# Performance work log

Measured on AMD Instinct MI355X. Metric: run time of the kernel, lower is better.

Reference implementation:

```python
import jax, jax.numpy as jnp
import numpy as np

B, L, M = 256, 8, 1024  # batch, input_length (= window), latent dim m
P = 8                   # predict_length


def setup_inputs() -> dict:
    key = jax.random.key(0)
    k1, k2, k3 = jax.random.split(key, 3)
    x = jax.random.normal(k1, (B, L, M), dtype=jnp.float32)
    # A initialized near identity (original init is torch.eye repeated), plus
    # small noise so the test is non-trivial and the recurrence stays stable.
    eye = jnp.broadcast_to(jnp.eye(M, dtype=jnp.float32), (L, M, M))
    A_real = eye / L + 0.02 * jax.random.normal(k2, (L, M, M), dtype=jnp.float32)
    A_imag = 0.02 * jax.random.normal(k3, (L, M, M), dtype=jnp.float32)
    return {"x": x, "A_real": A_real, "A_imag": A_imag, "predict_length": P}


def reference(x, A_real, A_imag, predict_length):
    # Complex DMD operator bank: A[j] is [M, M] cfloat.
    A = (A_real + 1j * A_imag).astype(jnp.complex64)
    Lw = x.shape[1]
    # Original inner loop: u2 += A[j] @ uc[:, -j]  (note -0 == 0!)
    #   j=0 pairs A[0] with window position 0; j>=1 pairs A[j] with position Lw-j.
    # Re-index so term for window position p uses Ag[p]: Ag[0]=A[0], Ag[p]=A[Lw-p].
    idx = jnp.concatenate([jnp.array([0]), jnp.arange(Lw - 1, 0, -1)])
    Ag = A[idx]  # [Lw, M, M]

    uc0 = x.astype(jnp.complex64)  # [B, Lw, M] sliding window state

    def step(uc, _):
        # Fused accumulation: sum_p Ag[p] @ uc[:, p]  -> [B, M]
        u2 = jnp.einsum("kmn,bkn->bm", Ag, uc)
        uc = jnp.concatenate([uc[:, 1:], u2[:, None]], axis=1)  # slide window
        return uc, None

    uc, _ = jax.lax.scan(step, uc0, None, length=predict_length)
    # Original casts cfloat -> double, which drops the imaginary part; keep fp32.
    return jnp.real(uc).astype(jnp.float32)
```

## Files before the change

### kernel.cpp

```cpp
#include <hip/hip_runtime.h>


#define LW 8

typedef __attribute__((ext_vector_type(8))) short  short8;
typedef __attribute__((ext_vector_type(8))) __bf16 bf16x8;
typedef __attribute__((ext_vector_type(4))) float  f32x4;
typedef __attribute__((ext_vector_type(4))) float  f4;
typedef const __attribute__((address_space(1))) void gvoid_t;
typedef __attribute__((address_space(3))) void lvoid_t;

static __device__ __forceinline__ short f2bf(float f) {
  unsigned u = __builtin_bit_cast(unsigned, f);
  u += 0x7FFFu + ((u >> 16) & 1u);
  return (short)(u >> 16);
}
static __device__ __forceinline__ float bf2f(short s) {
  unsigned u = ((unsigned)(unsigned short)s) << 16;
  return __builtin_bit_cast(float, u);
}
static __device__ __forceinline__ f32x4 mfma16(short8 a, short8 b, f32x4 c) {
  return __builtin_amdgcn_mfma_f32_16x16x32_bf16(
      __builtin_bit_cast(bf16x8, a), __builtin_bit_cast(bf16x8, b), c, 0, 0, 0);
}

__global__ __launch_bounds__(1024) void prep_all(const float* __restrict__ x,
                                                 const float* __restrict__ Ar,
                                                 const float* __restrict__ Ai,
                                                 short* __restrict__ Sr2,
                                                 short* __restrict__ Si2,
                                                 short* __restrict__ Wr5,
                                                 short* __restrict__ Wi5) {
  const int bid = blockIdx.x;
  if (bid < 1024) {
    const int tg = bid * 1024 + threadIdx.x;
    const int sq = tg & 3, col = (tg >> 2) & 31, kcg = (tg >> 7) & 31;
    const int colt = (tg >> 12) & 31, p = tg >> 17;
    const int qn = sq ^ ((col >> 1) & 3);
    const int m = (colt << 5) + col, n0 = (kcg << 5) + (qn << 3);
    const int qm = (LW - p) & 7;
    const size_t src = ((size_t)((qm << 10) + m) << 10) + n0;
    f4 r0 = *(const f4*)(Ar + src), r1 = *(const f4*)(Ar + src + 4);
    f4 i0 = *(const f4*)(Ai + src), i1 = *(const f4*)(Ai + src + 4);
    short8 vr, vi;
#pragma unroll
    for (int j = 0; j < 4; ++j) {
      vr[j] = f2bf(r0[j]); vr[j + 4] = f2bf(r1[j]);
      vi[j] = f2bf(i0[j]); vi[j + 4] = f2bf(i1[j]);
    }
    *(short8*)(Wr5 + ((size_t)tg << 3)) = vr;
    *(short8*)(Wi5 + ((size_t)tg << 3)) = vi;
  } else {
    const int tg = (bid - 1024) * 1024 + threadIdx.x;
    const int qn = tg & 3, kc = (tg >> 2) & 31, b = (tg >> 7) & 255, s = tg >> 15;
    const float* xp = x + ((size_t)(b * LW + s) << 10) + (kc << 5) + (qn << 3);
    f4 x0 = *(const f4*)xp, x1 = *(const f4*)(xp + 4);
    short8 v;
#pragma unroll
    for (int j = 0; j < 4; ++j) { v[j] = f2bf(x0[j]); v[j + 4] = f2bf(x1[j]); }
    const int sq = qn ^ ((b >> 1) & 3);
    const size_t dst = ((size_t)s << 18) + (kc << 13) + (b << 5) + (sq << 3);
    *(short8*)(Sr2 + dst) = v;
    short8 z = {0, 0, 0, 0, 0, 0, 0, 0};
    *(short8*)(Si2 + dst) = z;
  }
}


#define LOADA(set_, kc_) do {                                                    \
    const int kg_ = ((ks << 4) + (kc_)) << 13;                                   \
    _Pragma("unroll")                                                            \
    for (int rf_ = 0; rf_ < 4; ++rf_) {                                          \
      aR[set_][rf_] = *(const short8*)(SrB + kg_ + aoffG[rf_]);                  \
      aI[set_][rf_] = *(const short8*)(SiB + kg_ + aoffG[rf_]);                  \
    }                                                                            \
  } while (0)

#define COMP(set_, kc_) do {                                                     \
    short8 bR_[2], bI_[2];                                                       \
    _Pragma("unroll")                                                            \
    for (int cf_ = 0; cf_ < 2; ++cf_) {                                          \
      bR_[cf_] = *(const short8*)(ldsW + ((kc_) << 10) + boffL[cf_]);            \
      bI_[cf_] = *(const short8*)(ldsW + 16384 + ((kc_) << 10) + boffL[cf_]);    \
    }                                                                            \
    __builtin_amdgcn_s_setprio(1);                                               \
    _Pragma("unroll")                                                            \
    for (int rf_ = 0; rf_ < 4; ++rf_) {                                          \
      const short8 nI_ = aI[set_][rf_] ^ SGN;                                    \
      _Pragma("unroll")                                                          \
      for (int cf_ = 0; cf_ < 2; ++cf_) {                                        \
        accR[rf_][cf_] = mfma16(aR[set_][rf_], bR_[cf_], accR[rf_][cf_]);        \
        accR[rf_][cf_] = mfma16(nI_,           bI_[cf_], accR[rf_][cf_]);        \
        accI[rf_][cf_] = mfma16(aR[set_][rf_], bI_[cf_], accI[rf_][cf_]);        \
        accI[rf_][cf_] = mfma16(aI[set_][rf_], bR_[cf_], accI[rf_][cf_]);        \
      }                                                                          \
    }                                                                            \
    __builtin_amdgcn_s_setprio(0);                                               \
  } while (0)

__global__ __launch_bounds__(256, 2) void gemm_step(const short* __restrict__ Sr2,
                                                    const short* __restrict__ Si2,
                                                    const short* __restrict__ Wr5,
                                                    const short* __restrict__ Wi5,
                                                    short* __restrict__ Pp,
                                                    int t) {
  __shared__ short ldsW[32768];

  const int bid   = blockIdx.x;
  const int p     = bid & 7;
  const int inner = bid >> 3;
  const int colt  = inner & 31;
  const int ks    = inner >> 5;
  const int s     = (p + t) & 7;

  const int tid = threadIdx.x, lane = tid & 63, w = tid >> 6;
  const int l15 = lane & 15, q = lane >> 4;

  {
    const short* baseR = Wr5 + (((size_t)((p << 5) + colt)) << 15) + ((size_t)ks << 14);
    const short* baseI = Wi5 + (((size_t)((p << 5) + colt)) << 15) + ((size_t)ks << 14);
#pragma unroll
    for (int j = 0; j < 16; ++j) {
      const int gid  = (j << 8) + tid;
      const int arr  = gid >> 11;
      const int rem  = gid & 2047;
      const short* src = (arr ? baseI : baseR) + (rem << 3);
      __builtin_amdgcn_global_load_lds((gvoid_t*)src,
          (lvoid_t*)&ldsW[(arr << 14) + (rem << 3)], 16, 0, 0);
    }
  }

  const short* SrB = Sr2 + ((size_t)s << 18);
  const short* SiB = Si2 + ((size_t)s << 18);
  int aoffG[4], boffL[2];
#pragma unroll
  for (int rf = 0; rf < 4; ++rf) {
    const int row = (w << 6) + (rf << 4) + l15;
    aoffG[rf] = (row << 5) + ((q ^ ((row >> 1) & 3)) << 3);
  }
#pragma unroll
  for (int cf = 0; cf < 2; ++cf) {
    const int col = (cf << 4) + l15;
    boffL[cf] = (col << 5) + ((q ^ ((col >> 1) & 3)) << 3);
  }

  f32x4 accR[4][2], accI[4][2];
  const f32x4 z4 = {0.f, 0.f, 0.f, 0.f};
#pragma unroll
  for (int a = 0; a < 4; ++a)
#pragma unroll
    for (int c = 0; c < 2; ++c) { accR[a][c] = z4; accI[a][c] = z4; }

  const short8 SGN = {(short)0x8000, (short)0x8000, (short)0x8000, (short)0x8000,
                      (short)0x8000, (short)0x8000, (short)0x8000, (short)0x8000};

  short8 aR[2][4], aI[2][4];

  LOADA(0, 0);
  __syncthreads();

#pragma unroll
  for (int kc = 0; kc < 16; ++kc) {
    if (kc < 15) LOADA((kc + 1) & 1, kc + 1);
    COMP(kc & 1, kc);
  }

  short* op = Pp + ((size_t)(((((p << 1) + ks) << 5) + colt) << 3) << 11) + (tid << 3);
#pragma unroll
  for (int rf = 0; rf < 4; ++rf)
#pragma unroll
    for (int cf = 0; cf < 2; ++cf) {
      short8 sv;
#pragma unroll
      for (int rg = 0; rg < 4; ++rg) {
        sv[rg]     = f2bf(accR[rf][cf][rg]);
        sv[rg + 4] = f2bf(accI[rf][cf][rg]);
      }
      *(short8*)(op + ((size_t)((rf << 1) + cf) << 11)) = sv;
    }
}

__global__ __launch_bounds__(256) void reduce_step(const short* __restrict__ Pp,
                                                   short* __restrict__ Sr2,
                                                   short* __restrict__ Si2,
                                                   float* __restrict__ out,
                                                   int t) {
  const int r = blockIdx.x * 256 + threadIdx.x;
  const int tidg = r & 255, o = (r >> 8) & 7, colt = r >> 11;

  float sum[8] = {0.f, 0.f, 0.f, 0.f, 0.f, 0.f, 0.f, 0.f};
#pragma unroll
  for (int sl = 0; sl < 16; ++sl) {
    const short8 v = *(const short8*)(
        Pp + ((size_t)((((sl << 5) + colt) << 3) + o) << 11) + (tidg << 3));
#pragma unroll
    for (int jj = 0; jj < 8; ++jj) sum[jj] += bf2f(v[jj]);
  }

  const int rf = o >> 1, cf = o & 1;
  const int lane = tidg & 63, w = tidg >> 6;
  const int l15 = lane & 15, q = lane >> 4;
  const int row0 = (w << 6) + (rf << 4) + (q << 2);
  const int col  = (colt << 5) + (cf << 4) + l15;
  const int kc = col >> 5, qn = (col >> 3) & 3, j = col & 7;

#pragma unroll
  for (int rg = 0; rg < 4; ++rg) {
    const int row = row0 + rg;
    out[((size_t)((row << 3) + t) << 10) + col] = sum[rg];
    const int sq = qn ^ ((row >> 1) & 3);
    const size_t idx = ((size_t)t << 18) + (kc << 13) + (row << 5) + (sq << 3) + j;
    Sr2[idx] = f2bf(sum[rg]);
    Si2[idx] = f2bf(sum[rg + 4]);
  }
}

extern "C" void kernel_launch(void* const* d_in, const int* in_sizes, int n_in,
                              void* d_out, int out_size, void* d_ws, size_t ws_size,
                              hipStream_t stream) {
  const float* x  = (const float*)d_in[0];
  const float* Ar = (const float*)d_in[1];
  const float* Ai = (const float*)d_in[2];
  float* out = (float*)d_out;

  char* ws = (char*)d_ws;
  if (ws_size < (60u << 20)) return;
  short* Sr2 = (short*)(ws);
  short* Si2 = (short*)(ws + (4u  << 20));
  short* Wr5 = (short*)(ws + (8u  << 20));
  short* Wi5 = (short*)(ws + (24u << 20));
  short* Pp  = (short*)(ws + (40u << 20));

  prep_all<<<dim3(1280), dim3(1024), 0, stream>>>(x, Ar, Ai, Sr2, Si2, Wr5, Wi5);
  for (int t = 0; t < 8; ++t) {
    gemm_step<<<dim3(512), dim3(256), 0, stream>>>(Sr2, Si2, Wr5, Wi5, Pp, t);
    reduce_step<<<dim3(256), dim3(256), 0, stream>>>(Pp, Sr2, Si2, out, t);
  }
}
```

Measured before the change: 231.0 us.

## Drop split-K in gemm_step, use 16-column tiles over full K

Each gemm_step block now covers a 16-column output tile over the full K=1024 reduction instead of a 32-column tile over half of K. The weight layout in prep_all is re-tiled to match. The reduce stage now sums 8 partials instead of 16, so the partial-sum buffer and its traffic are halved. In exchange each block runs a longer serial K loop with fewer MFMAs per B-fragment load, and the A tiles are reloaded across twice as many column tiles.

```diff
diff --git a/kernel.cpp b/kernel.cpp
--- a/kernel.cpp
+++ b/kernel.cpp
@@ -1,5 +1,4 @@
 #include <hip/hip_runtime.h>
-
 
 #define LW 8
 
@@ -29,15 +28,15 @@
                                                  const float* __restrict__ Ai,
                                                  short* __restrict__ Sr2,
                                                  short* __restrict__ Si2,
-                                                 short* __restrict__ Wr5,
-                                                 short* __restrict__ Wi5) {
+                                                 short* __restrict__ Wr6,
+                                                 short* __restrict__ Wi6) {
   const int bid = blockIdx.x;
   if (bid < 1024) {
     const int tg = bid * 1024 + threadIdx.x;
-    const int sq = tg & 3, col = (tg >> 2) & 31, kcg = (tg >> 7) & 31;
-    const int colt = (tg >> 12) & 31, p = tg >> 17;
+    const int sq = tg & 3, col = (tg >> 2) & 15, kcg = (tg >> 6) & 31;
+    const int colt = (tg >> 11) & 63, p = tg >> 17;
     const int qn = sq ^ ((col >> 1) & 3);
-    const int m = (colt << 5) + col, n0 = (kcg << 5) + (qn << 3);
+    const int m = (colt << 4) + col, n0 = (kcg << 5) + (qn << 3);
     const int qm = (LW - p) & 7;
     const size_t src = ((size_t)((qm << 10) + m) << 10) + n0;
     f4 r0 = *(const f4*)(Ar + src), r1 = *(const f4*)(Ar + src + 4);
@@ -48,8 +47,8 @@
       vr[j] = f2bf(r0[j]); vr[j + 4] = f2bf(r1[j]);
       vi[j] = f2bf(i0[j]); vi[j + 4] = f2bf(i1[j]);
     }
-    *(short8*)(Wr5 + ((size_t)tg << 3)) = vr;
-    *(short8*)(Wi5 + ((size_t)tg << 3)) = vi;
+    *(short8*)(Wr6 + ((size_t)tg << 3)) = vr;
+    *(short8*)(Wi6 + ((size_t)tg << 3)) = vi;
   } else {
     const int tg = (bid - 1024) * 1024 + threadIdx.x;
     const int qn = tg & 3, kc = (tg >> 2) & 31, b = (tg >> 7) & 255, s = tg >> 15;
@@ -68,7 +67,7 @@
 
 
 #define LOADA(set_, kc_) do {                                                    \
-    const int kg_ = ((ks << 4) + (kc_)) << 13;                                   \
+    const int kg_ = (kc_) << 13;                                                 \
     _Pragma("unroll")                                                            \
     for (int rf_ = 0; rf_ < 4; ++rf_) {                                          \
       aR[set_][rf_] = *(const short8*)(SrB + kg_ + aoffG[rf_]);                  \
@@ -77,48 +76,39 @@
   } while (0)
 
 #define COMP(set_, kc_) do {                                                     \
-    short8 bR_[2], bI_[2];                                                       \
-    _Pragma("unroll")                                                            \
-    for (int cf_ = 0; cf_ < 2; ++cf_) {                                          \
-      bR_[cf_] = *(const short8*)(ldsW + ((kc_) << 10) + boffL[cf_]);            \
-      bI_[cf_] = *(const short8*)(ldsW + 16384 + ((kc_) << 10) + boffL[cf_]);    \
-    }                                                                            \
+    const short8 bR_ = *(const short8*)(ldsW + ((kc_) << 9) + boffL0);           \
+    const short8 bI_ = *(const short8*)(ldsW + 16384 + ((kc_) << 9) + boffL0);   \
     __builtin_amdgcn_s_setprio(1);                                               \
     _Pragma("unroll")                                                            \
     for (int rf_ = 0; rf_ < 4; ++rf_) {                                          \
       const short8 nI_ = aI[set_][rf_] ^ SGN;                                    \
-      _Pragma("unroll")                                                          \
-      for (int cf_ = 0; cf_ < 2; ++cf_) {                                        \
-        accR[rf_][cf_] = mfma16(aR[set_][rf_], bR_[cf_], accR[rf_][cf_]);        \
-        accR[rf_][cf_] = mfma16(nI_,           bI_[cf_], accR[rf_][cf_]);        \
-        accI[rf_][cf_] = mfma16(aR[set_][rf_], bI_[cf_], accI[rf_][cf_]);        \
-        accI[rf_][cf_] = mfma16(aI[set_][rf_], bR_[cf_], accI[rf_][cf_]);        \
-      }                                                                          \
+      accR[rf_] = mfma16(aR[set_][rf_], bR_, accR[rf_]);                         \
+      accR[rf_] = mfma16(nI_,           bI_, accR[rf_]);                         \
+      accI[rf_] = mfma16(aR[set_][rf_], bI_, accI[rf_]);                         \
+      accI[rf_] = mfma16(aI[set_][rf_], bR_, accI[rf_]);                         \
     }                                                                            \
     __builtin_amdgcn_s_setprio(0);                                               \
   } while (0)
 
 __global__ __launch_bounds__(256, 2) void gemm_step(const short* __restrict__ Sr2,
                                                     const short* __restrict__ Si2,
-                                                    const short* __restrict__ Wr5,
-                                                    const short* __restrict__ Wi5,
+                                                    const short* __restrict__ Wr6,
+                                                    const short* __restrict__ Wi6,
                                                     short* __restrict__ Pp,
                                                     int t) {
   __shared__ short ldsW[32768];
 
-  const int bid   = blockIdx.x;
-  const int p     = bid & 7;
-  const int inner = bid >> 3;
-  const int colt  = inner & 31;
-  const int ks    = inner >> 5;
-  const int s     = (p + t) & 7;
+  const int bid  = blockIdx.x;
+  const int p    = bid & 7;
+  const int colt = bid >> 3;
+  const int s    = (p + t) & 7;
 
   const int tid = threadIdx.x, lane = tid & 63, w = tid >> 6;
   const int l15 = lane & 15, q = lane >> 4;
 
   {
-    const short* baseR = Wr5 + (((size_t)((p << 5) + colt)) << 15) + ((size_t)ks << 14);
-    const short* baseI = Wi5 + (((size_t)((p << 5) + colt)) << 15) + ((size_t)ks << 14);
+    const short* baseR = Wr6 + (((size_t)((p << 6) + colt)) << 14);
+    const short* baseI = Wi6 + (((size_t)((p << 6) + colt)) << 14);
 #pragma unroll
     for (int j = 0; j < 16; ++j) {
       const int gid  = (j << 8) + tid;
@@ -132,24 +122,18 @@
 
   const short* SrB = Sr2 + ((size_t)s << 18);
   const short* SiB = Si2 + ((size_t)s << 18);
-  int aoffG[4], boffL[2];
+  int aoffG[4];
 #pragma unroll
   for (int rf = 0; rf < 4; ++rf) {
     const int row = (w << 6) + (rf << 4) + l15;
     aoffG[rf] = (row << 5) + ((q ^ ((row >> 1) & 3)) << 3);
   }
-#pragma unroll
-  for (int cf = 0; cf < 2; ++cf) {
-    const int col = (cf << 4) + l15;
-    boffL[cf] = (col << 5) + ((q ^ ((col >> 1) & 3)) << 3);
-  }
-
-  f32x4 accR[4][2], accI[4][2];
+  const int boffL0 = (l15 << 5) + ((q ^ ((l15 >> 1) & 3)) << 3);
+
+  f32x4 accR[4], accI[4];
   const f32x4 z4 = {0.f, 0.f, 0.f, 0.f};
 #pragma unroll
-  for (int a = 0; a < 4; ++a)
-#pragma unroll
-    for (int c = 0; c < 2; ++c) { accR[a][c] = z4; accI[a][c] = z4; }
+  for (int a = 0; a < 4; ++a) { accR[a] = z4; accI[a] = z4; }
 
   const short8 SGN = {(short)0x8000, (short)0x8000, (short)0x8000, (short)0x8000,
                       (short)0x8000, (short)0x8000, (short)0x8000, (short)0x8000};
@@ -160,24 +144,22 @@
   __syncthreads();
 
 #pragma unroll
-  for (int kc = 0; kc < 16; ++kc) {
-    if (kc < 15) LOADA((kc + 1) & 1, kc + 1);
+  for (int kc = 0; kc < 32; ++kc) {
+    if (kc < 31) LOADA((kc + 1) & 1, kc + 1);
     COMP(kc & 1, kc);
   }
 
-  short* op = Pp + ((size_t)(((((p << 1) + ks) << 5) + colt) << 3) << 11) + (tid << 3);
-#pragma unroll
-  for (int rf = 0; rf < 4; ++rf)
-#pragma unroll
-    for (int cf = 0; cf < 2; ++cf) {
-      short8 sv;
-#pragma unroll
-      for (int rg = 0; rg < 4; ++rg) {
-        sv[rg]     = f2bf(accR[rf][cf][rg]);
-        sv[rg + 4] = f2bf(accI[rf][cf][rg]);
-      }
-      *(short8*)(op + ((size_t)((rf << 1) + cf) << 11)) = sv;
+  short* op = Pp + ((size_t)(((p << 6) + colt) << 2) << 11) + (tid << 3);
+#pragma unroll
+  for (int rf = 0; rf < 4; ++rf) {
+    short8 sv;
+#pragma unroll
+    for (int rg = 0; rg < 4; ++rg) {
+      sv[rg]     = f2bf(accR[rf][rg]);
+      sv[rg + 4] = f2bf(accI[rf][rg]);
     }
+    *(short8*)(op + ((size_t)rf << 11)) = sv;
+  }
 }
 
 __global__ __launch_bounds__(256) void reduce_step(const short* __restrict__ Pp,
@@ -186,22 +168,21 @@
                                                    float* __restrict__ out,
                                                    int t) {
   const int r = blockIdx.x * 256 + threadIdx.x;
-  const int tidg = r & 255, o = (r >> 8) & 7, colt = r >> 11;
+  const int tidg = r & 255, rf = (r >> 8) & 3, colt = r >> 10;
 
   float sum[8] = {0.f, 0.f, 0.f, 0.f, 0.f, 0.f, 0.f, 0.f};
 #pragma unroll
-  for (int sl = 0; sl < 16; ++sl) {
+  for (int sl = 0; sl < 8; ++sl) {
     const short8 v = *(const short8*)(
-        Pp + ((size_t)((((sl << 5) + colt) << 3) + o) << 11) + (tidg << 3));
+        Pp + ((size_t)((((sl << 6) + colt) << 2) + rf) << 11) + (tidg << 3));
 #pragma unroll
     for (int jj = 0; jj < 8; ++jj) sum[jj] += bf2f(v[jj]);
   }
 
-  const int rf = o >> 1, cf = o & 1;
   const int lane = tidg & 63, w = tidg >> 6;
   const int l15 = lane & 15, q = lane >> 4;
   const int row0 = (w << 6) + (rf << 4) + (q << 2);
-  const int col  = (colt << 5) + (cf << 4) + l15;
+  const int col  = (colt << 4) + l15;
   const int kc = col >> 5, qn = (col >> 3) & 3, j = col & 7;
 
 #pragma unroll
@@ -224,16 +205,16 @@
   float* out = (float*)d_out;
 
   char* ws = (char*)d_ws;
-  if (ws_size < (60u << 20)) return;
+  if (ws_size < (52u << 20)) return;
   short* Sr2 = (short*)(ws);
   short* Si2 = (short*)(ws + (4u  << 20));
-  short* Wr5 = (short*)(ws + (8u  << 20));
-  short* Wi5 = (short*)(ws + (24u << 20));
+  short* Wr6 = (short*)(ws + (8u  << 20));
+  short* Wi6 = (short*)(ws + (24u << 20));
   short* Pp  = (short*)(ws + (40u << 20));
 
-  prep_all<<<dim3(1280), dim3(1024), 0, stream>>>(x, Ar, Ai, Sr2, Si2, Wr5, Wi5);
+  prep_all<<<dim3(1280), dim3(1024), 0, stream>>>(x, Ar, Ai, Sr2, Si2, Wr6, Wi6);
   for (int t = 0; t < 8; ++t) {
-    gemm_step<<<dim3(512), dim3(256), 0, stream>>>(Sr2, Si2, Wr5, Wi5, Pp, t);
+    gemm_step<<<dim3(512), dim3(256), 0, stream>>>(Sr2, Si2, Wr6, Wi6, Pp, t);
     reduce_step<<<dim3(256), dim3(256), 0, stream>>>(Pp, Sr2, Si2, out, t);
   }
 }
```

Measured after the change: 260.4 us. 1.13x slower.
